# Kernel optimization log

Hardware: AMD Instinct MI355X
Metric: run time of the kernel (lower is better)

## Reference

```python
import jax, jax.numpy as jnp
import numpy as np

N_NODES = 50000
D_IN = 256
D_OUT = 128
N_POS = 1600000   # positive edges used for GCN aggregation
N_PRED = 500000   # edges to score


def setup_inputs() -> dict:
    key = jax.random.key(0)
    ks = jax.random.split(key, 6)
    x = jax.random.normal(ks[0], (N_NODES, D_IN), dtype=jnp.float32)
    pos_edge_index = jax.random.randint(ks[1], (2, N_POS), 0, N_NODES)
    edge_index = jax.random.randint(ks[2], (2, N_PRED), 0, N_NODES)
    # init_linear: Linear(d_in, d_in); stored as (in, out) so fwd is x @ W1 + b1
    W1 = jax.random.normal(ks[3], (D_IN, D_IN), dtype=jnp.float32) / np.sqrt(D_IN).astype(np.float32)
    b1 = jnp.zeros((D_IN,), dtype=jnp.float32)
    # GCNConv weight (in, out) and bias
    Wc = jax.random.normal(ks[4], (D_IN, D_OUT), dtype=jnp.float32) / np.sqrt(D_IN).astype(np.float32)
    bc = jnp.zeros((D_OUT,), dtype=jnp.float32)
    return dict(x=x, edge_index=edge_index, pos_edge_index=pos_edge_index,
                W1=W1, b1=b1, Wc=Wc, bc=bc)


def reference(x, edge_index, pos_edge_index, W1, b1, Wc, bc):
    n = x.shape[0]
    # init_linear
    h = x @ W1 + b1                                  # [N, D_IN]
    # GCNConv: linear transform first, then normalized scatter-add aggregation
    h = h @ Wc                                       # [N, D_OUT]
    # add self-loops (PyG GCNConv default add_self_loops=True, edge_weight=1)
    loops = jnp.arange(n, dtype=pos_edge_index.dtype)
    row = jnp.concatenate([pos_edge_index[0], loops])  # source
    col = jnp.concatenate([pos_edge_index[1], loops])  # target (aggregation)
    # symmetric normalization: deg over target, norm = d^-1/2[row]*d^-1/2[col]
    deg = jax.ops.segment_sum(jnp.ones_like(col, dtype=h.dtype), col, num_segments=n)
    dinv = jnp.where(deg > 0, jax.lax.rsqrt(deg), 0.0)
    norm = dinv[row] * dinv[col]                     # [E+N]
    msgs = h[row] * norm[:, None]                    # gather + scale
    out = jax.ops.segment_sum(msgs, col, num_segments=n) + bc  # scatter-add + bias
    # edge dot-product scoring
    logits = (out[edge_index[0]] * out[edge_index[1]]).sum(axis=-1)  # [N_PRED]
    return logits
```

## Files before the change

kernel.cpp:

```cpp
#include <hip/hip_runtime.h>

#define N_NODES 50000
#define D_IN 256
#define D_OUT 128
#define N_POS 1600000
#define N_PRED 500000

#define G_BUCKETS 782
#define GPAD 1024
#define SB 160
#define CHUNK 10000
#define CAP 4096

typedef __attribute__((ext_vector_type(8))) short short8;
typedef __attribute__((ext_vector_type(4))) float f32x4;

__device__ __forceinline__ unsigned short f2bf(float f) {
    unsigned int u = __float_as_uint(f);
    u += 0x7FFFu + ((u >> 16) & 1u);
    return (unsigned short)(u >> 16);
}
__device__ __forceinline__ unsigned int pk2(float a, float b) {
    unsigned int ua = __float_as_uint(a), ub = __float_as_uint(b);
    ua += 0x7FFFu + ((ua >> 16) & 1u);
    ub += 0x7FFFu + ((ub >> 16) & 1u);
    return (ua >> 16) | (ub & 0xFFFF0000u);
}
__device__ __forceinline__ float bflo(unsigned int u) { return __uint_as_float(u << 16); }
__device__ __forceinline__ float bfhi(unsigned int u) { return __uint_as_float(u & 0xFFFF0000u); }

__global__ void fuse_weights_k(const float* __restrict__ W1, const float* __restrict__ Wc,
                               const float* __restrict__ b1,
                               unsigned short* __restrict__ Bp, float* __restrict__ bf) {
    int gid = blockIdx.x * blockDim.x + threadIdx.x;
    int k = gid >> 7;
    int n = gid & 127;
    float acc = 0.f;
    #pragma unroll 4
    for (int kk = 0; kk < D_IN; ++kk)
        acc += W1[k * D_IN + kk] * Wc[kk * D_OUT + n];
    int ks = k >> 5, q = (k >> 3) & 3, jj = k & 7;
    int nt = n >> 4, nl = n & 15;
    int lane = q * 16 + nl;
    Bp[(((long)(ks * 8 + nt)) * 64 + lane) * 8 + jj] = f2bf(acc);
    if (gid < D_OUT) {
        float accb = 0.f;
        for (int kk = 0; kk < D_IN; ++kk)
            accb += b1[kk] * Wc[kk * D_OUT + gid];
        bf[gid] = accb;
    }
}

__global__ void init_fill_k(int* __restrict__ bfill) {
    int g = blockIdx.x * blockDim.x + threadIdx.x;
    if (g < G_BUCKETS) bfill[g] = g * CAP;
}

__global__ __launch_bounds__(256) void bucket_scatter_k(const int* __restrict__ row,
                                                        const int* __restrict__ col,
                                                        int* __restrict__ bfill,
                                                        unsigned int* __restrict__ eb) {
    __shared__ int hist[GPAD];
    __shared__ int lofs[GPAD];
    __shared__ int fill2[GPAD];
    __shared__ int base[GPAD];
    __shared__ int part[256];
    __shared__ unsigned int stag[CHUNK];
    int t = threadIdx.x;
    for (int i = t; i < GPAD; i += 256) { hist[i] = 0; fill2[i] = 0; }
    __syncthreads();
    int e0 = blockIdx.x * CHUNK;
    for (int i = t; i < CHUNK; i += 256)
        atomicAdd(&hist[col[e0 + i] >> 6], 1);
    __syncthreads();
    int h[4], p4 = 0;
    #pragma unroll
    for (int i = 0; i < 4; ++i) { h[i] = hist[4 * t + i]; p4 += h[i]; }
    part[t] = p4;
    __syncthreads();
    for (int d = 1; d < 256; d <<= 1) {
        int add = (t >= d) ? part[t - d] : 0;
        __syncthreads();
        part[t] += add;
        __syncthreads();
    }
    int ex = part[t] - p4;
    #pragma unroll
    for (int i = 0; i < 4; ++i) { lofs[4 * t + i] = ex; ex += h[i]; }
    __syncthreads();
    for (int g = t; g < G_BUCKETS; g += 256) {
        int c = hist[g];
        base[g] = c ? atomicAdd(&bfill[g], c) : 0;
    }
    for (int i = t; i < CHUNK; i += 256) {
        int c = col[e0 + i];
        int g = c >> 6;
        unsigned int u = (unsigned int)row[e0 + i] | ((unsigned int)(c & 63) << 16)
                       | ((unsigned int)g << 22);
        int lp = atomicAdd(&fill2[g], 1);
        stag[lofs[g] + lp] = u;
    }
    __syncthreads();
    for (int i = t; i < CHUNK; i += 256) {
        unsigned int u = stag[i];
        int g = u >> 22;
        eb[base[g] + (i - lofs[g])] = u;
    }
}

__global__ __launch_bounds__(256) void csr_build_k(const int* __restrict__ bfill,
                                                   const unsigned int* __restrict__ eb,
                                                   unsigned short* __restrict__ csr,
                                                   int* __restrict__ offs,
                                                   int* __restrict__ ends,
                                                   float* __restrict__ dinv) {
    __shared__ unsigned int stag[CAP];
    __shared__ unsigned short stag2[CAP];
    __shared__ int hist[64], lofs[64], fill[64];
    int t = threadIdx.x;
    int g = blockIdx.x;
    int s = g * CAP;
    int cnt = bfill[g] - s;
    if (t < 64) { hist[t] = 0; fill[t] = 0; }
    __syncthreads();
    for (int i = t; i < cnt; i += 256) {
        unsigned int u = eb[s + i];
        stag[i] = u;
        atomicAdd(&hist[(u >> 16) & 63], 1);
    }
    __syncthreads();
    if (t == 0) {
        int run = 0;
        for (int k = 0; k < 64; ++k) { lofs[k] = run; run += hist[k]; }
    }
    __syncthreads();
    if (t < 64) {
        int v = g * 64 + t;
        if (v < N_NODES) {
            offs[v] = s + lofs[t];
            ends[v] = s + lofs[t] + hist[t];
            dinv[v] = rsqrtf((float)hist[t] + 1.0f);
        }
    }
    for (int i = t; i < cnt; i += 256) {
        unsigned int u = stag[i];
        int nl = (u >> 16) & 63;
        int lp = atomicAdd(&fill[nl], 1);
        stag2[lofs[nl] + lp] = (unsigned short)(u & 0xFFFF);
    }
    __syncthreads();
    for (int i = t; i < cnt; i += 256)
        csr[s + i] = stag2[i];
}

__global__ __launch_bounds__(256) void gemm_mfma_k(const float* __restrict__ x,
                                                   const uint4* __restrict__ Bp,
                                                   const float* __restrict__ bf,
                                                   const float* __restrict__ dinv,
                                                   unsigned short* __restrict__ hsb) {
    __shared__ unsigned short ot[4][16 * 128];
    const int wave = threadIdx.x >> 6;
    const int lane = threadIdx.x & 63;
    const int q    = lane >> 4;
    const int ml   = lane & 15;
    const int m0   = blockIdx.x * 64 + wave * 16;

    f32x4 acc[8];
    #pragma unroll
    for (int t = 0; t < 8; ++t) acc[t] = (f32x4){0.f, 0.f, 0.f, 0.f};

    long arow = m0 + ml; if (arow > N_NODES - 1) arow = N_NODES - 1;
    const float* xrow = x + arow * D_IN + q * 8;

    #pragma unroll
    for (int ks = 0; ks < 8; ++ks) {
        float4 xa = *(const float4*)(xrow + ks * 32);
        float4 xb = *(const float4*)(xrow + ks * 32 + 4);
        union { short8 s; unsigned int u[4]; } af;
        af.u[0] = pk2(xa.x, xa.y);
        af.u[1] = pk2(xa.z, xa.w);
        af.u[2] = pk2(xb.x, xb.y);
        af.u[3] = pk2(xb.z, xb.w);
        #pragma unroll
        for (int nt = 0; nt < 8; ++nt) {
            union { uint4 v; short8 s; } bu;
            bu.v = Bp[(long)(ks * 8 + nt) * 64 + lane];
            acc[nt] = __builtin_amdgcn_mfma_f32_16x16x32_bf16(af.s, bu.s, acc[nt], 0, 0, 0);
        }
    }

    float dv[4];
    #pragma unroll
    for (int r = 0; r < 4; ++r) {
        int v = m0 + q * 4 + r;
        dv[r] = dinv[v > N_NODES - 1 ? N_NODES - 1 : v];
    }
    unsigned short* o = ot[wave];
    #pragma unroll
    for (int nt = 0; nt < 8; ++nt) {
        float bn = bf[nt * 16 + ml];
        #pragma unroll
        for (int r = 0; r < 4; ++r) {
            float val = dv[r] * (acc[nt][r] + bn);
            o[(q * 4 + r) * 128 + nt * 16 + ml] = f2bf(val);
        }
    }
    __syncthreads();
    #pragma unroll
    for (int i = 0; i < 4; ++i) {
        int fb = i * 1024 + lane * 16;
        int v = m0 + (fb >> 8);
        if (v < N_NODES) {
            uint4 val = *(const uint4*)((const char*)o + fb);
            *(uint4*)((char*)hsb + (long)v * 256 + (fb & 255)) = val;
        }
    }
}

__global__ __launch_bounds__(256) void aggregate_csr_k(const int* __restrict__ offs,
                                                       const int* __restrict__ ends,
                                                       const unsigned short* __restrict__ csr,
                                                       const uint4* __restrict__ hs4,
                                                       const float* __restrict__ dinv,
                                                       const float* __restrict__ bc,
                                                       uint4* __restrict__ feat4) {
    int v    = blockIdx.x * 4 + (threadIdx.x >> 6);
    int lane = threadIdx.x & 63;
    int grp  = lane >> 4, li = lane & 15;
    int s0 = offs[v], s1 = ends[v];

    float a[8] = {0.f, 0.f, 0.f, 0.f, 0.f, 0.f, 0.f, 0.f};
    int i = s0 + grp;
    for (; i + 4 < s1; i += 8) {
        int r0 = csr[i], r1 = csr[i + 4];
        uint4 u0 = hs4[r0 * 16 + li];
        uint4 u1 = hs4[r1 * 16 + li];
        a[0] += bflo(u0.x) + bflo(u1.x);  a[1] += bfhi(u0.x) + bfhi(u1.x);
        a[2] += bflo(u0.y) + bflo(u1.y);  a[3] += bfhi(u0.y) + bfhi(u1.y);
        a[4] += bflo(u0.z) + bflo(u1.z);  a[5] += bfhi(u0.z) + bfhi(u1.z);
        a[6] += bflo(u0.w) + bflo(u1.w);  a[7] += bfhi(u0.w) + bfhi(u1.w);
    }
    if (i < s1) {
        uint4 u = hs4[(int)csr[i] * 16 + li];
        a[0] += bflo(u.x); a[1] += bfhi(u.x);
        a[2] += bflo(u.y); a[3] += bfhi(u.y);
        a[4] += bflo(u.z); a[5] += bfhi(u.z);
        a[6] += bflo(u.w); a[7] += bfhi(u.w);
    }
    #pragma unroll
    for (int j = 0; j < 8; ++j) {
        a[j] += __shfl_xor(a[j], 16);
        a[j] += __shfl_xor(a[j], 32);
    }
    if (grp == 0) {
        uint4 su = hs4[v * 16 + li];
        float dv = dinv[v];
        float4 b0 = *(const float4*)(bc + li * 8);
        float4 b1 = *(const float4*)(bc + li * 8 + 4);
        float f0 = dv * (a[0] + bflo(su.x)) + b0.x;
        float f1 = dv * (a[1] + bfhi(su.x)) + b0.y;
        float f2 = dv * (a[2] + bflo(su.y)) + b0.z;
        float f3 = dv * (a[3] + bfhi(su.y)) + b0.w;
        float f4 = dv * (a[4] + bflo(su.z)) + b1.x;
        float f5 = dv * (a[5] + bfhi(su.z)) + b1.y;
        float f6 = dv * (a[6] + bflo(su.w)) + b1.z;
        float f7 = dv * (a[7] + bfhi(su.w)) + b1.w;
        uint4 o;
        o.x = pk2(f0, f1); o.y = pk2(f2, f3); o.z = pk2(f4, f5); o.w = pk2(f6, f7);
        feat4[v * 16 + li] = o;
    }
}

__global__ void score_k(const int* __restrict__ src, const int* __restrict__ dst,
                        const uint4* __restrict__ feat4, float* __restrict__ out) {
    int gid = blockIdx.x * blockDim.x + threadIdx.x;
    int e = gid >> 4;
    int c = gid & 15;
    if (e >= N_PRED) return;
    int a = src[e], b = dst[e];
    uint4 ua = feat4[(long)a * 16 + c];
    uint4 ub = feat4[(long)b * 16 + c];
    float p = bflo(ua.x) * bflo(ub.x) + bfhi(ua.x) * bfhi(ub.x)
            + bflo(ua.y) * bflo(ub.y) + bfhi(ua.y) * bfhi(ub.y)
            + bflo(ua.z) * bflo(ub.z) + bfhi(ua.z) * bfhi(ub.z)
            + bflo(ua.w) * bflo(ub.w) + bfhi(ua.w) * bfhi(ub.w);
    #pragma unroll
    for (int m = 8; m; m >>= 1) p += __shfl_xor(p, m, 16);
    if (c == 0) out[e] = p;
}

extern "C" void kernel_launch(void* const* d_in, const int* in_sizes, int n_in,
                              void* d_out, int out_size, void* d_ws, size_t ws_size,
                              hipStream_t stream) {
    const float* x   = (const float*)d_in[0];
    const int*   ei  = (const int*)  d_in[1];
    const int*   pe  = (const int*)  d_in[2];
    const float* W1  = (const float*)d_in[3];
    const float* b1  = (const float*)d_in[4];
    const float* Wc  = (const float*)d_in[5];
    const float* bc  = (const float*)d_in[6];
    float* out = (float*)d_out;

    const int* pe_row = pe;
    const int* pe_col = pe + N_POS;
    const int* ei_src = ei;
    const int* ei_dst = ei + N_PRED;

    char* w = (char*)d_ws;
    unsigned short* Bp = (unsigned short*)w;  w += 32768 * 2;
    float* bf    = (float*)w;                 w += 128 * 4;
    float* dinv  = (float*)w;                 w += 50000 * 4;
    int*   bfill = (int*)w;                   w += GPAD * 4;
    int*   offs  = (int*)w;                   w += 50000 * 4;
    int*   ends  = (int*)w;                   w += 50000 * 4;
    unsigned int* eb = (unsigned int*)w;      w += (long)G_BUCKETS * CAP * 4;
    unsigned short* csr = (unsigned short*)w; w += (long)G_BUCKETS * CAP * 2;
    unsigned short* hsb   = (unsigned short*)w;  w += (long)N_NODES * D_OUT * 2;
    unsigned short* featb = (unsigned short*)w;

    init_fill_k     <<<4, 256, 0, stream>>>(bfill);
    bucket_scatter_k<<<SB, 256, 0, stream>>>(pe_row, pe_col, bfill, eb);
    csr_build_k     <<<G_BUCKETS, 256, 0, stream>>>(bfill, eb, csr, offs, ends, dinv);

    fuse_weights_k<<<128, 256, 0, stream>>>(W1, Wc, b1, Bp, bf);
    gemm_mfma_k   <<<(N_NODES + 63) / 64, 256, 0, stream>>>(x, (const uint4*)Bp, bf, dinv, hsb);

    aggregate_csr_k<<<N_NODES / 4, 256, 0, stream>>>(offs, ends, csr, (const uint4*)hsb,
                                                     dinv, bc, (uint4*)featb);

    score_k       <<<(int)(((long)N_PRED * 16) / 256), 256, 0, stream>>>(
                      ei_src, ei_dst, (const uint4*)featb, out);
}
```

Before: 279.2 us.

## Merge edge bucketing with GEMM in one launch and defer source normalization

```diff
diff --git a/kernel.cpp b/kernel.cpp
--- a/kernel.cpp
+++ b/kernel.cpp
@@ -8,9 +8,10 @@
 
 #define G_BUCKETS 782
 #define GPAD 1024
-#define SB 160
-#define CHUNK 10000
+#define SB 640
+#define CHUNK 2500
 #define CAP 4096
+#define GEMM_BLOCKS 782
 
 typedef __attribute__((ext_vector_type(8))) short short8;
 typedef __attribute__((ext_vector_type(4))) float f32x4;
@@ -31,7 +32,12 @@
 
 __global__ void fuse_weights_k(const float* __restrict__ W1, const float* __restrict__ Wc,
                                const float* __restrict__ b1,
-                               unsigned short* __restrict__ Bp, float* __restrict__ bf) {
+                               unsigned short* __restrict__ Bp, float* __restrict__ bf,
+                               int* __restrict__ bfill) {
+    if (blockIdx.x == 128) {
+        for (int g = threadIdx.x; g < G_BUCKETS; g += 256) bfill[g] = g * CAP;
+        return;
+    }
     int gid = blockIdx.x * blockDim.x + threadIdx.x;
     int k = gid >> 7;
     int n = gid & 127;
@@ -51,60 +57,113 @@
     }
 }
 
-__global__ void init_fill_k(int* __restrict__ bfill) {
-    int g = blockIdx.x * blockDim.x + threadIdx.x;
-    if (g < G_BUCKETS) bfill[g] = g * CAP;
-}
-
-__global__ __launch_bounds__(256) void bucket_scatter_k(const int* __restrict__ row,
-                                                        const int* __restrict__ col,
-                                                        int* __restrict__ bfill,
-                                                        unsigned int* __restrict__ eb) {
-    __shared__ int hist[GPAD];
-    __shared__ int lofs[GPAD];
-    __shared__ int fill2[GPAD];
-    __shared__ int base[GPAD];
-    __shared__ int part[256];
-    __shared__ unsigned int stag[CHUNK];
-    int t = threadIdx.x;
-    for (int i = t; i < GPAD; i += 256) { hist[i] = 0; fill2[i] = 0; }
-    __syncthreads();
-    int e0 = blockIdx.x * CHUNK;
-    for (int i = t; i < CHUNK; i += 256)
-        atomicAdd(&hist[col[e0 + i] >> 6], 1);
-    __syncthreads();
-    int h[4], p4 = 0;
-    #pragma unroll
-    for (int i = 0; i < 4; ++i) { h[i] = hist[4 * t + i]; p4 += h[i]; }
-    part[t] = p4;
-    __syncthreads();
-    for (int d = 1; d < 256; d <<= 1) {
-        int add = (t >= d) ? part[t - d] : 0;
-        __syncthreads();
-        part[t] += add;
-        __syncthreads();
-    }
-    int ex = part[t] - p4;
-    #pragma unroll
-    for (int i = 0; i < 4; ++i) { lofs[4 * t + i] = ex; ex += h[i]; }
-    __syncthreads();
-    for (int g = t; g < G_BUCKETS; g += 256) {
-        int c = hist[g];
-        base[g] = c ? atomicAdd(&bfill[g], c) : 0;
-    }
-    for (int i = t; i < CHUNK; i += 256) {
-        int c = col[e0 + i];
-        int g = c >> 6;
-        unsigned int u = (unsigned int)row[e0 + i] | ((unsigned int)(c & 63) << 16)
-                       | ((unsigned int)g << 22);
-        int lp = atomicAdd(&fill2[g], 1);
-        stag[lofs[g] + lp] = u;
-    }
-    __syncthreads();
-    for (int i = t; i < CHUNK; i += 256) {
-        unsigned int u = stag[i];
-        int g = u >> 22;
-        eb[base[g] + (i - lofs[g])] = u;
+__global__ __launch_bounds__(256) void scatter_gemm_k(const int* __restrict__ row,
+                                                      const int* __restrict__ col,
+                                                      int* __restrict__ bfill,
+                                                      unsigned int* __restrict__ eb,
+                                                      const float* __restrict__ x,
+                                                      const uint4* __restrict__ Bp,
+                                                      const float* __restrict__ bf,
+                                                      unsigned short* __restrict__ hsb) {
+    __shared__ __align__(16) char smem[27456];
+    if (blockIdx.x < GEMM_BLOCKS) {
+        const int wave = threadIdx.x >> 6;
+        const int lane = threadIdx.x & 63;
+        const int q    = lane >> 4;
+        const int ml   = lane & 15;
+        const int m0   = blockIdx.x * 64 + wave * 16;
+
+        f32x4 acc[8];
+        #pragma unroll
+        for (int t = 0; t < 8; ++t) acc[t] = (f32x4){0.f, 0.f, 0.f, 0.f};
+
+        long arow = m0 + ml; if (arow > N_NODES - 1) arow = N_NODES - 1;
+        const float* xrow = x + arow * D_IN + q * 8;
+
+        #pragma unroll
+        for (int ks = 0; ks < 8; ++ks) {
+            float4 xa = *(const float4*)(xrow + ks * 32);
+            float4 xb = *(const float4*)(xrow + ks * 32 + 4);
+            union { short8 s; unsigned int u[4]; } af;
+            af.u[0] = pk2(xa.x, xa.y);
+            af.u[1] = pk2(xa.z, xa.w);
+            af.u[2] = pk2(xb.x, xb.y);
+            af.u[3] = pk2(xb.z, xb.w);
+            #pragma unroll
+            for (int nt = 0; nt < 8; ++nt) {
+                union { uint4 v; short8 s; } bu;
+                bu.v = Bp[(long)(ks * 8 + nt) * 64 + lane];
+                acc[nt] = __builtin_amdgcn_mfma_f32_16x16x32_bf16(af.s, bu.s, acc[nt], 0, 0, 0);
+            }
+        }
+
+        unsigned short* o = (unsigned short*)smem + wave * 2048;
+        #pragma unroll
+        for (int nt = 0; nt < 8; ++nt) {
+            float bn = bf[nt * 16 + ml];
+            #pragma unroll
+            for (int r = 0; r < 4; ++r) {
+                float val = acc[nt][r] + bn;
+                o[(q * 4 + r) * 128 + nt * 16 + ml] = f2bf(val);
+            }
+        }
+        __syncthreads();
+        #pragma unroll
+        for (int i = 0; i < 4; ++i) {
+            int fb = i * 1024 + lane * 16;
+            int v = m0 + (fb >> 8);
+            if (v < N_NODES) {
+                uint4 val = *(const uint4*)((const char*)o + fb);
+                *(uint4*)((char*)hsb + (long)v * 256 + (fb & 255)) = val;
+            }
+        }
+    } else {
+        int* hist  = (int*)smem;
+        int* lofs  = hist + GPAD;
+        int* fill2 = lofs + GPAD;
+        int* base  = fill2 + GPAD;
+        int* part  = base + GPAD;
+        unsigned int* stag = (unsigned int*)(part + 256);
+        int t = threadIdx.x;
+        for (int i = t; i < GPAD; i += 256) { hist[i] = 0; fill2[i] = 0; }
+        __syncthreads();
+        int e0 = (blockIdx.x - GEMM_BLOCKS) * CHUNK;
+        for (int i = t; i < CHUNK; i += 256)
+            atomicAdd(&hist[col[e0 + i] >> 6], 1);
+        __syncthreads();
+        int h[4], p4 = 0;
+        #pragma unroll
+        for (int i = 0; i < 4; ++i) { h[i] = hist[4 * t + i]; p4 += h[i]; }
+        part[t] = p4;
+        __syncthreads();
+        for (int d = 1; d < 256; d <<= 1) {
+            int add = (t >= d) ? part[t - d] : 0;
+            __syncthreads();
+            part[t] += add;
+            __syncthreads();
+        }
+        int ex = part[t] - p4;
+        #pragma unroll
+        for (int i = 0; i < 4; ++i) { lofs[4 * t + i] = ex; ex += h[i]; }
+        __syncthreads();
+        for (int g = t; g < G_BUCKETS; g += 256) {
+            int c = hist[g];
+            base[g] = c ? atomicAdd(&bfill[g], c) : 0;
+        }
+        for (int i = t; i < CHUNK; i += 256) {
+            int c = col[e0 + i];
+            int g = c >> 6;
+            unsigned int u = (unsigned int)row[e0 + i] | ((unsigned int)(c & 63) << 16)
+                           | ((unsigned int)g << 22);
+            int lp = atomicAdd(&fill2[g], 1);
+            stag[lofs[g] + lp] = u;
+        }
+        __syncthreads();
+        for (int i = t; i < CHUNK; i += 256) {
+            unsigned int u = stag[i];
+            int g = u >> 22;
+            eb[base[g] + (i - lofs[g])] = u;
+        }
     }
 }
 
@@ -153,70 +212,6 @@
         csr[s + i] = stag2[i];
 }
 
-__global__ __launch_bounds__(256) void gemm_mfma_k(const float* __restrict__ x,
-                                                   const uint4* __restrict__ Bp,
-                                                   const float* __restrict__ bf,
-                                                   const float* __restrict__ dinv,
-                                                   unsigned short* __restrict__ hsb) {
-    __shared__ unsigned short ot[4][16 * 128];
-    const int wave = threadIdx.x >> 6;
-    const int lane = threadIdx.x & 63;
-    const int q    = lane >> 4;
-    const int ml   = lane & 15;
-    const int m0   = blockIdx.x * 64 + wave * 16;
-
-    f32x4 acc[8];
-    #pragma unroll
-    for (int t = 0; t < 8; ++t) acc[t] = (f32x4){0.f, 0.f, 0.f, 0.f};
-
-    long arow = m0 + ml; if (arow > N_NODES - 1) arow = N_NODES - 1;
-    const float* xrow = x + arow * D_IN + q * 8;
-
-    #pragma unroll
-    for (int ks = 0; ks < 8; ++ks) {
-        float4 xa = *(const float4*)(xrow + ks * 32);
-        float4 xb = *(const float4*)(xrow + ks * 32 + 4);
-        union { short8 s; unsigned int u[4]; } af;
-        af.u[0] = pk2(xa.x, xa.y);
-        af.u[1] = pk2(xa.z, xa.w);
-        af.u[2] = pk2(xb.x, xb.y);
-        af.u[3] = pk2(xb.z, xb.w);
-        #pragma unroll
-        for (int nt = 0; nt < 8; ++nt) {
-            union { uint4 v; short8 s; } bu;
-            bu.v = Bp[(long)(ks * 8 + nt) * 64 + lane];
-            acc[nt] = __builtin_amdgcn_mfma_f32_16x16x32_bf16(af.s, bu.s, acc[nt], 0, 0, 0);
-        }
-    }
-
-    float dv[4];
-    #pragma unroll
-    for (int r = 0; r < 4; ++r) {
-        int v = m0 + q * 4 + r;
-        dv[r] = dinv[v > N_NODES - 1 ? N_NODES - 1 : v];
-    }
-    unsigned short* o = ot[wave];
-    #pragma unroll
-    for (int nt = 0; nt < 8; ++nt) {
-        float bn = bf[nt * 16 + ml];
-        #pragma unroll
-        for (int r = 0; r < 4; ++r) {
-            float val = dv[r] * (acc[nt][r] + bn);
-            o[(q * 4 + r) * 128 + nt * 16 + ml] = f2bf(val);
-        }
-    }
-    __syncthreads();
-    #pragma unroll
-    for (int i = 0; i < 4; ++i) {
-        int fb = i * 1024 + lane * 16;
-        int v = m0 + (fb >> 8);
-        if (v < N_NODES) {
-            uint4 val = *(const uint4*)((const char*)o + fb);
-            *(uint4*)((char*)hsb + (long)v * 256 + (fb & 255)) = val;
-        }
-    }
-}
-
 __global__ __launch_bounds__(256) void aggregate_csr_k(const int* __restrict__ offs,
                                                        const int* __restrict__ ends,
                                                        const unsigned short* __restrict__ csr,
@@ -235,17 +230,24 @@
         int r0 = csr[i], r1 = csr[i + 4];
         uint4 u0 = hs4[r0 * 16 + li];
         uint4 u1 = hs4[r1 * 16 + li];
-        a[0] += bflo(u0.x) + bflo(u1.x);  a[1] += bfhi(u0.x) + bfhi(u1.x);
-        a[2] += bflo(u0.y) + bflo(u1.y);  a[3] += bfhi(u0.y) + bfhi(u1.y);
-        a[4] += bflo(u0.z) + bflo(u1.z);  a[5] += bfhi(u0.z) + bfhi(u1.z);
-        a[6] += bflo(u0.w) + bflo(u1.w);  a[7] += bfhi(u0.w) + bfhi(u1.w);
+        float d0 = dinv[r0], d1 = dinv[r1];
+        a[0] = fmaf(d0, bflo(u0.x), a[0]); a[0] = fmaf(d1, bflo(u1.x), a[0]);
+        a[1] = fmaf(d0, bfhi(u0.x), a[1]); a[1] = fmaf(d1, bfhi(u1.x), a[1]);
+        a[2] = fmaf(d0, bflo(u0.y), a[2]); a[2] = fmaf(d1, bflo(u1.y), a[2]);
+        a[3] = fmaf(d0, bfhi(u0.y), a[3]); a[3] = fmaf(d1, bfhi(u1.y), a[3]);
+        a[4] = fmaf(d0, bflo(u0.z), a[4]); a[4] = fmaf(d1, bflo(u1.z), a[4]);
+        a[5] = fmaf(d0, bfhi(u0.z), a[5]); a[5] = fmaf(d1, bfhi(u1.z), a[5]);
+        a[6] = fmaf(d0, bflo(u0.w), a[6]); a[6] = fmaf(d1, bflo(u1.w), a[6]);
+        a[7] = fmaf(d0, bfhi(u0.w), a[7]); a[7] = fmaf(d1, bfhi(u1.w), a[7]);
     }
     if (i < s1) {
-        uint4 u = hs4[(int)csr[i] * 16 + li];
-        a[0] += bflo(u.x); a[1] += bfhi(u.x);
-        a[2] += bflo(u.y); a[3] += bfhi(u.y);
-        a[4] += bflo(u.z); a[5] += bfhi(u.z);
-        a[6] += bflo(u.w); a[7] += bfhi(u.w);
+        int r = csr[i];
+        uint4 u = hs4[r * 16 + li];
+        float d = dinv[r];
+        a[0] = fmaf(d, bflo(u.x), a[0]); a[1] = fmaf(d, bfhi(u.x), a[1]);
+        a[2] = fmaf(d, bflo(u.y), a[2]); a[3] = fmaf(d, bfhi(u.y), a[3]);
+        a[4] = fmaf(d, bflo(u.z), a[4]); a[5] = fmaf(d, bfhi(u.z), a[5]);
+        a[6] = fmaf(d, bflo(u.w), a[6]); a[7] = fmaf(d, bfhi(u.w), a[7]);
     }
     #pragma unroll
     for (int j = 0; j < 8; ++j) {
@@ -257,14 +259,14 @@
         float dv = dinv[v];
         float4 b0 = *(const float4*)(bc + li * 8);
         float4 b1 = *(const float4*)(bc + li * 8 + 4);
-        float f0 = dv * (a[0] + bflo(su.x)) + b0.x;
-        float f1 = dv * (a[1] + bfhi(su.x)) + b0.y;
-        float f2 = dv * (a[2] + bflo(su.y)) + b0.z;
-        float f3 = dv * (a[3] + bfhi(su.y)) + b0.w;
-        float f4 = dv * (a[4] + bflo(su.z)) + b1.x;
-        float f5 = dv * (a[5] + bfhi(su.z)) + b1.y;
-        float f6 = dv * (a[6] + bflo(su.w)) + b1.z;
-        float f7 = dv * (a[7] + bfhi(su.w)) + b1.w;
+        float f0 = dv * (a[0] + dv * bflo(su.x)) + b0.x;
+        float f1 = dv * (a[1] + dv * bfhi(su.x)) + b0.y;
+        float f2 = dv * (a[2] + dv * bflo(su.y)) + b0.z;
+        float f3 = dv * (a[3] + dv * bfhi(su.y)) + b0.w;
+        float f4 = dv * (a[4] + dv * bflo(su.z)) + b1.x;
+        float f5 = dv * (a[5] + dv * bfhi(su.z)) + b1.y;
+        float f6 = dv * (a[6] + dv * bflo(su.w)) + b1.z;
+        float f7 = dv * (a[7] + dv * bfhi(su.w)) + b1.w;
         uint4 o;
         o.x = pk2(f0, f1); o.y = pk2(f2, f3); o.z = pk2(f4, f5); o.w = pk2(f6, f7);
         feat4[v * 16 + li] = o;
@@ -318,12 +320,12 @@
     unsigned short* hsb   = (unsigned short*)w;  w += (long)N_NODES * D_OUT * 2;
     unsigned short* featb = (unsigned short*)w;
 
-    init_fill_k     <<<4, 256, 0, stream>>>(bfill);
-    bucket_scatter_k<<<SB, 256, 0, stream>>>(pe_row, pe_col, bfill, eb);
-    csr_build_k     <<<G_BUCKETS, 256, 0, stream>>>(bfill, eb, csr, offs, ends, dinv);
-
-    fuse_weights_k<<<128, 256, 0, stream>>>(W1, Wc, b1, Bp, bf);
-    gemm_mfma_k   <<<(N_NODES + 63) / 64, 256, 0, stream>>>(x, (const uint4*)Bp, bf, dinv, hsb);
+    fuse_weights_k<<<129, 256, 0, stream>>>(W1, Wc, b1, Bp, bf, bfill);
+
+    scatter_gemm_k<<<GEMM_BLOCKS + SB, 256, 0, stream>>>(pe_row, pe_col, bfill, eb,
+                                                         x, (const uint4*)Bp, bf, hsb);
+
+    csr_build_k   <<<G_BUCKETS, 256, 0, stream>>>(bfill, eb, csr, offs, ends, dinv);
 
     aggregate_csr_k<<<N_NODES / 4, 256, 0, stream>>>(offs, ends, csr, (const uint4*)hsb,
                                                      dinv, bc, (uint4*)featb);
```

New measurement: 267.8 us. 4.1% less time.
